# Kernel optimization log

Hardware: AMD Instinct MI355X
Metric: run time of the kernel (lower is better)

Reference implementation:

```python
import jax, jax.numpy as jnp
import numpy as np

BN_EPS = 1e-5


def gcn_conv(x, src, dst, ew, W, b, n_nodes):
    # PyG GCNConv: xW, then D^-1/2 (A+I) D^-1/2 aggregation (self-loop weight 1), then +bias
    xw = x @ W                                                  # [N, out]
    deg = jax.ops.segment_sum(ew, dst, num_segments=n_nodes) + 1.0  # includes self-loop
    dinv = jax.lax.rsqrt(deg)                                   # [N]
    norm = dinv[src] * ew * dinv[dst]                           # [E]
    agg = jax.ops.segment_sum(xw[src] * norm[:, None], dst, num_segments=n_nodes)
    agg = agg + xw * (1.0 / deg)[:, None]                       # self-loop term: dinv_i*1*dinv_i = 1/deg_i
    return agg + b


def batch_norm(h, gamma, beta):
    # training-mode BatchNorm1d: batch statistics (biased variance)
    mean = jnp.mean(h, axis=0)
    var = jnp.mean((h - mean) ** 2, axis=0)
    return (h - mean) * jax.lax.rsqrt(var + BN_EPS) * gamma + beta


def setup_inputs() -> dict:
    key = jax.random.key(0)
    ks = jax.random.split(key, 12)
    N, E, F_IN, H1, H2 = 100000, 1600000, 128, 64, 32
    x = jax.random.normal(ks[0], (N, F_IN), dtype=jnp.float32)
    edge_index = jax.random.randint(ks[1], (2, E), 0, N, dtype=jnp.int64)
    edge_weight = jax.random.uniform(ks[2], (E,), dtype=jnp.float32)
    W1 = jax.random.normal(ks[3], (F_IN, H1), dtype=jnp.float32) / np.sqrt(F_IN)
    b1 = jnp.zeros((H1,), dtype=jnp.float32)
    W2 = jax.random.normal(ks[4], (H1, H2), dtype=jnp.float32) / np.sqrt(H1)
    b2 = jnp.zeros((H2,), dtype=jnp.float32)
    g1 = jnp.ones((H1,), dtype=jnp.float32)
    be1 = jnp.zeros((H1,), dtype=jnp.float32)
    g2 = jnp.ones((H2,), dtype=jnp.float32)
    be2 = jnp.zeros((H2,), dtype=jnp.float32)
    Wl = jax.random.normal(ks[5], (H2, 1), dtype=jnp.float32) / np.sqrt(H2)
    bl = jnp.zeros((1,), dtype=jnp.float32)
    return {"x": x, "edge_index": edge_index, "edge_weight": edge_weight,
            "W1": W1, "b1": b1, "g1": g1, "be1": be1,
            "W2": W2, "b2": b2, "g2": g2, "be2": be2,
            "Wl": Wl, "bl": bl}


def reference(x, edge_index, edge_weight, W1, b1, g1, be1, W2, b2, g2, be2, Wl, bl):
    n_nodes = x.shape[0]
    src, dst = edge_index[0], edge_index[1]
    h = gcn_conv(x, src, dst, edge_weight, W1, b1, n_nodes)
    h = jax.nn.relu(batch_norm(h, g1, be1))          # dropout = identity (eval)
    h = gcn_conv(h, src, dst, edge_weight, W2, b2, n_nodes)
    h = jax.nn.relu(batch_norm(h, g2, be2))
    return (h @ Wl + bl).squeeze(-1)                 # [N]
```

## Files before the change

### kernel.cpp

```cpp
#include <hip/hip_runtime.h>
#include <hip/hip_bf16.h>

#define FIN 128
#define C1 64
#define C2 32
#define BN_EPS 1e-5f
#define CAP 28
#define OVFCAP 65536
#define R1 16
#define R2 16

typedef __hip_bfloat16 bf16;

__global__ __launch_bounds__(256) void k_fillpad(const int* __restrict__ ei, int* __restrict__ pcnt,
                                                 int* __restrict__ pad, int* __restrict__ ovf,
                                                 int* __restrict__ ovfn, int E) {
  int e = blockIdx.x * 256 + threadIdx.x;
  if (e < E) {
    int dst = ei[E + e];
    int pos = atomicAdd(&pcnt[dst], 1);
    if (pos < CAP) {
      pad[(size_t)dst * CAP + pos] = e;
    } else {
      int oi = atomicAdd(ovfn, 1);
      if (oi < OVFCAP) ovf[oi] = e;
    }
  }
}

__global__ __launch_bounds__(256) void k_ovfdeg(const int* __restrict__ ovf, const int* __restrict__ ovfn,
                                                const int* __restrict__ ei, const float* __restrict__ ew,
                                                float* __restrict__ deg, int E) {
  int n = ovfn[0];
  n = n < OVFCAP ? n : OVFCAP;
  for (int i = blockIdx.x * 256 + threadIdx.x; i < n; i += gridDim.x * 256) {
    int eid = ovf[i];
    atomicAdd(&deg[ei[E + eid]], ew[eid]);
  }
}

__global__ __launch_bounds__(256) void k_degdinv(const int* __restrict__ pcnt, const int* __restrict__ pad,
                                                 const float* __restrict__ ew, float* __restrict__ deg, int N) {
  int i = blockIdx.x * 256 + threadIdx.x;
  if (i < N) {
    int c = pcnt[i];
    c = c < CAP ? c : CAP;
    float s = deg[i] + 1.0f;
    const int* row = pad + (size_t)i * CAP;
    for (int k = 0; k < c; ++k) s += ew[row[k]];
    deg[i] = rsqrtf(s);
  }
}

__global__ __launch_bounds__(256) void k_gemm1(const float* __restrict__ x, const float* __restrict__ W1,
                                               bf16* __restrict__ xw1, int N) {
  const int lane = threadIdx.x & 63;
  const int w = threadIdx.x >> 6;
  float wr[32];
#pragma unroll
  for (int kk = 0; kk < 32; ++kk) wr[kk] = W1[(32 * w + kk) * C1 + lane];
  __shared__ float xs[R1][FIN];
  __shared__ float part[R1][4][C1];
  for (int base = blockIdx.x * R1; base < N; base += gridDim.x * R1) {
    int nrows = min(R1, N - base);
    __syncthreads();
    for (int t = threadIdx.x; t < nrows * FIN; t += 256) {
      int r = t >> 7, k = t & 127;
      xs[r][k] = x[(size_t)(base + r) * FIN + k];
    }
    __syncthreads();
#pragma unroll 4
    for (int r = 0; r < R1; ++r) {
      if (r >= nrows) break;
      const float* xrow = &xs[r][32 * w];
      float acc = 0.f;
#pragma unroll
      for (int kk = 0; kk < 32; kk += 4) {
        float4 xv = *(const float4*)&xrow[kk];
        acc = fmaf(xv.x, wr[kk], acc);
        acc = fmaf(xv.y, wr[kk + 1], acc);
        acc = fmaf(xv.z, wr[kk + 2], acc);
        acc = fmaf(xv.w, wr[kk + 3], acc);
      }
      part[r][w][lane] = acc;
    }
    __syncthreads();
    for (int t = threadIdx.x; t < nrows * C1; t += 256) {
      int r = t >> 6, c = t & 63;
      float v = (part[r][0][c] + part[r][1][c]) + (part[r][2][c] + part[r][3][c]);
      xw1[(size_t)(base + r) * C1 + c] = __float2bfloat16(v);
    }
  }
}

__global__ __launch_bounds__(256) void k_agg1(const int* __restrict__ pcnt, const int* __restrict__ pad,
                                              const int* __restrict__ ei, const float* __restrict__ ew,
                                              const float* __restrict__ dinv, const bf16* __restrict__ xw,
                                              const float* __restrict__ b, float* __restrict__ h, int N, int E) {
  const int lane = threadIdx.x & 63;
  const int wid = (blockIdx.x * 256 + threadIdx.x) >> 6;
  const int nw = (gridDim.x * 256) >> 6;
  for (int dst = wid; dst < N; dst += nw) {
    float dv = dinv[dst];
    float acc = fmaf(__bfloat162float(xw[(size_t)dst * C1 + lane]), dv * dv, b[lane]);
    int c = pcnt[dst];
    c = c < CAP ? c : CAP;
    int sv = 0;
    float nv = 0.f;
    if (lane < c) {
      int eid = pad[(size_t)dst * CAP + lane];
      sv = ei[eid];
      nv = dinv[sv] * ew[eid] * dv;
    }
    for (int k = 0; k < c; ++k) {
      int s = __shfl(sv, k);
      float nm = __shfl(nv, k);
      acc = fmaf(__bfloat162float(xw[(size_t)s * C1 + lane]), nm, acc);
    }
    h[(size_t)dst * C1 + lane] = acc;
  }
}

__global__ __launch_bounds__(256) void k_ovf1(const int* __restrict__ ovf, const int* __restrict__ ovfn,
                                              const int* __restrict__ ei, const float* __restrict__ ew,
                                              const float* __restrict__ dinv, const bf16* __restrict__ xw,
                                              float* __restrict__ h, int E) {
  const int lane = threadIdx.x & 63;
  const int wid = (blockIdx.x * 256 + threadIdx.x) >> 6;
  const int nw = (gridDim.x * 256) >> 6;
  int n = ovfn[0];
  n = n < OVFCAP ? n : OVFCAP;
  for (int i = wid; i < n; i += nw) {
    int eid = ovf[i];
    int src = ei[eid];
    int dst = ei[E + eid];
    float nrm = dinv[src] * ew[eid] * dinv[dst];
    atomicAdd(&h[(size_t)dst * C1 + lane], __bfloat162float(xw[(size_t)src * C1 + lane]) * nrm);
  }
}

__global__ __launch_bounds__(256) void k_agg2(const int* __restrict__ pcnt, const int* __restrict__ pad,
                                              const int* __restrict__ ei, const float* __restrict__ ew,
                                              const float* __restrict__ dinv, const float* __restrict__ xw,
                                              const float* __restrict__ b, float* __restrict__ h, int N, int E) {
  const int lane = threadIdx.x & 63;
  const int j = lane & 31, sub = lane >> 5;
  const int wid = (blockIdx.x * 256 + threadIdx.x) >> 6;
  const int nw = (gridDim.x * 256) >> 6;
  for (int dst = wid; dst < N; dst += nw) {
    float dv = dinv[dst];
    float acc = (sub == 0) ? fmaf(xw[(size_t)dst * C2 + j], dv * dv, b[j]) : 0.f;
    int c = pcnt[dst];
    c = c < CAP ? c : CAP;
    int sv = 0;
    float nv = 0.f;
    if (lane < c) {
      int eid = pad[(size_t)dst * CAP + lane];
      sv = ei[eid];
      nv = dinv[sv] * ew[eid] * dv;
    }
    for (int k = sub; k < c; k += 2) {
      int s = __shfl(sv, k);
      float nm = __shfl(nv, k);
      acc = fmaf(xw[(size_t)s * C2 + j], nm, acc);
    }
    acc += __shfl_xor(acc, 32);
    if (sub == 0) h[(size_t)dst * C2 + j] = acc;
  }
}

__global__ __launch_bounds__(256) void k_ovf2(const int* __restrict__ ovf, const int* __restrict__ ovfn,
                                              const int* __restrict__ ei, const float* __restrict__ ew,
                                              const float* __restrict__ dinv, const float* __restrict__ xw,
                                              float* __restrict__ h, int E) {
  const int lane = threadIdx.x & 63;
  const int wid = (blockIdx.x * 256 + threadIdx.x) >> 6;
  const int nw = (gridDim.x * 256) >> 6;
  int n = ovfn[0];
  n = n < OVFCAP ? n : OVFCAP;
  for (int i = wid; i < n; i += nw) {
    int eid = ovf[i];
    int src = ei[eid];
    int dst = ei[E + eid];
    float nrm = dinv[src] * ew[eid] * dinv[dst];
    if (lane < C2) atomicAdd(&h[(size_t)dst * C2 + lane], xw[(size_t)src * C2 + lane] * nrm);
  }
}

template <int C>
__global__ __launch_bounds__(256) void k_bnstats(const float* __restrict__ h, float* __restrict__ stat, int N) {
  const int rpb = 256 / C;
  const int j = threadIdx.x % C;
  const int rloc = threadIdx.x / C;
  float s = 0.f, sq = 0.f;
  for (int r = blockIdx.x * rpb + rloc; r < N; r += gridDim.x * rpb) {
    float v = h[(size_t)r * C + j];
    s += v;
    sq = fmaf(v, v, sq);
  }
  __shared__ float ls[256], lq[256];
  ls[threadIdx.x] = s;
  lq[threadIdx.x] = sq;
  __syncthreads();
  if (threadIdx.x < C) {
    float ts = 0.f, tq = 0.f;
#pragma unroll
    for (int k = 0; k < rpb; ++k) {
      ts += ls[k * C + j];
      tq += lq[k * C + j];
    }
    atomicAdd(&stat[j], ts);
    atomicAdd(&stat[C + j], tq);
  }
}

template <int C>
__global__ void k_bnfinal(const float* __restrict__ stat, const float* __restrict__ g,
                          const float* __restrict__ be, float* __restrict__ ss, int N) {
  int j = threadIdx.x;
  if (j < C) {
    float inv_n = 1.0f / (float)N;
    float mean = stat[j] * inv_n;
    float var = stat[C + j] * inv_n - mean * mean;
    float sc = g[j] * rsqrtf(var + BN_EPS);
    ss[j] = sc;
    ss[C + j] = be[j] - mean * sc;
  }
}

__global__ __launch_bounds__(256) void k_gemm2(const float* __restrict__ h1, const float* __restrict__ ss,
                                               const float* __restrict__ W2, float* __restrict__ xw2, int N) {
  const int lane = threadIdx.x & 63;
  const int w = threadIdx.x >> 6;
  const int c = lane & 31, hh = lane >> 5;
  const int slice = w * 2 + hh;
  float wr[8];
#pragma unroll
  for (int kk = 0; kk < 8; ++kk) wr[kk] = W2[(8 * slice + kk) * C2 + c];
  __shared__ float sss[2 * C1];
  if (threadIdx.x < 2 * C1) sss[threadIdx.x] = ss[threadIdx.x];
  __shared__ float xs[R2][C1];
  __shared__ float part[R2][8][C2];
  for (int base = blockIdx.x * R2; base < N; base += gridDim.x * R2) {
    int nrows = min(R2, N - base);
    __syncthreads();
    for (int t = threadIdx.x; t < nrows * C1; t += 256) {
      int r = t >> 6, k = t & 63;
      float v = fmaf(h1[(size_t)(base + r) * C1 + k], sss[k], sss[C1 + k]);
      xs[r][k] = v > 0.f ? v : 0.f;
    }
    __syncthreads();
#pragma unroll 4
    for (int r = 0; r < R2; ++r) {
      if (r >= nrows) break;
      const float* xrow = &xs[r][8 * slice];
      float4 a = *(const float4*)&xrow[0];
      float4 bb = *(const float4*)&xrow[4];
      float acc = a.x * wr[0];
      acc = fmaf(a.y, wr[1], acc);
      acc = fmaf(a.z, wr[2], acc);
      acc = fmaf(a.w, wr[3], acc);
      acc = fmaf(bb.x, wr[4], acc);
      acc = fmaf(bb.y, wr[5], acc);
      acc = fmaf(bb.z, wr[6], acc);
      acc = fmaf(bb.w, wr[7], acc);
      part[r][slice][c] = acc;
    }
    __syncthreads();
    for (int t = threadIdx.x; t < nrows * C2; t += 256) {
      int r = t >> 5, cc = t & 31;
      float v = 0.f;
#pragma unroll
      for (int s = 0; s < 8; ++s) v += part[r][s][cc];
      xw2[(size_t)(base + r) * C2 + cc] = v;
    }
  }
}

__global__ __launch_bounds__(256) void k_head(const float* __restrict__ h2, const float* __restrict__ ss,
                                              const float* __restrict__ Wl, const float* __restrict__ bl,
                                              float* __restrict__ out, int N) {
  const int lane = threadIdx.x & 63;
  const int j = lane & 31, sub = lane >> 5;
  const int wid = (blockIdx.x * 256 + threadIdx.x) >> 6;
  const int nw = (gridDim.x * 256) >> 6;
  const float sc = ss[j], sh = ss[C2 + j];
  const float wv = Wl[j];
  const float blv = bl[0];
  for (int r0 = wid * 2; r0 < N; r0 += nw * 2) {
    int row = r0 + sub;
    float v = 0.f;
    if (row < N) {
      float hh = fmaf(h2[(size_t)row * C2 + j], sc, sh);
      hh = hh > 0.f ? hh : 0.f;
      v = hh * wv;
    }
    v += __shfl_down(v, 16, 32);
    v += __shfl_down(v, 8, 32);
    v += __shfl_down(v, 4, 32);
    v += __shfl_down(v, 2, 32);
    v += __shfl_down(v, 1, 32);
    if (j == 0 && row < N) out[row] = v + blv;
  }
}

extern "C" void kernel_launch(void* const* d_in, const int* in_sizes, int n_in,
                              void* d_out, int out_size, void* d_ws, size_t ws_size,
                              hipStream_t stream) {
  const float* x = (const float*)d_in[0];
  const int* ei = (const int*)d_in[1];
  const float* ew = (const float*)d_in[2];
  const float* W1 = (const float*)d_in[3];
  const float* b1 = (const float*)d_in[4];
  const float* g1 = (const float*)d_in[5];
  const float* be1 = (const float*)d_in[6];
  const float* W2 = (const float*)d_in[7];
  const float* b2 = (const float*)d_in[8];
  const float* g2 = (const float*)d_in[9];
  const float* be2 = (const float*)d_in[10];
  const float* Wl = (const float*)d_in[11];
  const float* bl = (const float*)d_in[12];
  float* out = (float*)d_out;

  const int N = in_sizes[0] / FIN;
  const int E = in_sizes[2];

  float* Wf = (float*)d_ws;
  float* dinv = Wf;
  int* pcnt = (int*)(Wf + N);
  int* ovfn = (int*)(Wf + 2 * (size_t)N);
  float* stat1 = Wf + 2 * (size_t)N + 8;
  float* ss1 = stat1 + 128;
  float* stat2 = ss1 + 128;
  float* ss2 = stat2 + 64;
  int* ovf = (int*)(Wf + 2 * (size_t)N + 512);
  int* pad = ovf + OVFCAP;
  bf16* xw1 = (bf16*)(pad + (size_t)N * CAP);
  float* bufB = (float*)(xw1 + (size_t)N * C1);
  float* h1 = bufB;
  float* xw2 = (float*)xw1;
  float* h2 = bufB;

  hipMemsetAsync(Wf, 0, ((size_t)2 * N + 512) * sizeof(float), stream);

  k_fillpad<<<(E + 255) / 256, 256, 0, stream>>>(ei, pcnt, pad, ovf, ovfn, E);
  k_ovfdeg<<<16, 256, 0, stream>>>(ovf, ovfn, ei, ew, dinv, E);
  k_degdinv<<<(N + 255) / 256, 256, 0, stream>>>(pcnt, pad, ew, dinv, N);

  k_gemm1<<<2048, 256, 0, stream>>>(x, W1, xw1, N);
  k_agg1<<<4096, 256, 0, stream>>>(pcnt, pad, ei, ew, dinv, xw1, b1, h1, N, E);
  k_ovf1<<<256, 256, 0, stream>>>(ovf, ovfn, ei, ew, dinv, xw1, h1, E);
  k_bnstats<C1><<<1024, 256, 0, stream>>>(h1, stat1, N);
  k_bnfinal<C1><<<1, C1, 0, stream>>>(stat1, g1, be1, ss1, N);

  k_gemm2<<<2048, 256, 0, stream>>>(h1, ss1, W2, xw2, N);
  k_agg2<<<2048, 256, 0, stream>>>(pcnt, pad, ei, ew, dinv, xw2, b2, h2, N, E);
  k_ovf2<<<256, 256, 0, stream>>>(ovf, ovfn, ei, ew, dinv, xw2, h2, E);
  k_bnstats<C2><<<1024, 256, 0, stream>>>(h2, stat2, N);
  k_bnfinal<C2><<<1, C2, 0, stream>>>(stat2, g2, be2, ss2, N);

  k_head<<<1024, 256, 0, stream>>>(h2, ss2, Wl, bl, out, N);
}
```

Baseline: 650.7 us.

## Fuse edge bucketing with first GEMM and fold BN finalize into consumers

Merges the edge-to-destination padding kernel and the first dense GEMM into one launch, with disjoint block ranges doing each job so the atomic-heavy fill can overlap the compute-bound GEMM. The fill blocks now each scan all edges but only handle destinations in one of eight node ranges, which should improve atomic locality at the cost of reading the edge list eight times. The two single-block BN finalize kernels are removed, and the scale/shift computation is redone inside gemm2 and the head kernel, which saves launches but repeats a little work in every block.

```diff
diff --git a/kernel.cpp b/kernel.cpp
--- a/kernel.cpp
+++ b/kernel.cpp
@@ -9,21 +9,72 @@
 #define OVFCAP 65536
 #define R1 16
 #define R2 16
+#define GF 512
+#define GG 1024
 
 typedef __hip_bfloat16 bf16;
 
-__global__ __launch_bounds__(256) void k_fillpad(const int* __restrict__ ei, int* __restrict__ pcnt,
-                                                 int* __restrict__ pad, int* __restrict__ ovf,
-                                                 int* __restrict__ ovfn, int E) {
-  int e = blockIdx.x * 256 + threadIdx.x;
-  if (e < E) {
-    int dst = ei[E + e];
-    int pos = atomicAdd(&pcnt[dst], 1);
-    if (pos < CAP) {
-      pad[(size_t)dst * CAP + pos] = e;
-    } else {
-      int oi = atomicAdd(ovfn, 1);
-      if (oi < OVFCAP) ovf[oi] = e;
+__global__ __launch_bounds__(256) void k_fill_gemm1(const int* __restrict__ ei, int* __restrict__ pcnt,
+                                                    int* __restrict__ pad, int* __restrict__ ovf,
+                                                    int* __restrict__ ovfn,
+                                                    const float* __restrict__ x, const float* __restrict__ W1,
+                                                    bf16* __restrict__ xw1, int N, int E) {
+  __shared__ float xs[R1][FIN];
+  __shared__ float part[R1][4][C1];
+  if (blockIdx.x < GF) {
+    const int g = blockIdx.x & 7;
+    const int sub = blockIdx.x >> 3;
+    const int nsub = GF >> 3;
+    const int lo = (int)(((long long)N * g) >> 3);
+    const int hi = (int)(((long long)N * (g + 1)) >> 3);
+    for (int e = sub * 256 + threadIdx.x; e < E; e += nsub * 256) {
+      int dst = ei[E + e];
+      if (dst >= lo && dst < hi) {
+        int pos = atomicAdd(&pcnt[dst], 1);
+        if (pos < CAP) {
+          pad[(size_t)dst * CAP + pos] = e;
+        } else {
+          int oi = atomicAdd(ovfn, 1);
+          if (oi < OVFCAP) ovf[oi] = e;
+        }
+      }
+    }
+  } else {
+    const int bg = blockIdx.x - GF;
+    const int lane = threadIdx.x & 63;
+    const int w = threadIdx.x >> 6;
+    float wr[32];
+#pragma unroll
+    for (int kk = 0; kk < 32; ++kk) wr[kk] = W1[(32 * w + kk) * C1 + lane];
+    for (int base = bg * R1; base < N; base += GG * R1) {
+      int nrows = min(R1, N - base);
+      __syncthreads();
+      for (int t = threadIdx.x; t < nrows * FIN; t += 256) {
+        int r = t >> 7, k = t & 127;
+        xs[r][k] = x[(size_t)(base + r) * FIN + k];
+      }
+      __syncthreads();
+#pragma unroll 4
+      for (int r = 0; r < R1; ++r) {
+        if (r >= nrows) break;
+        const float* xrow = &xs[r][32 * w];
+        float acc = 0.f;
+#pragma unroll
+        for (int kk = 0; kk < 32; kk += 4) {
+          float4 xv = *(const float4*)&xrow[kk];
+          acc = fmaf(xv.x, wr[kk], acc);
+          acc = fmaf(xv.y, wr[kk + 1], acc);
+          acc = fmaf(xv.z, wr[kk + 2], acc);
+          acc = fmaf(xv.w, wr[kk + 3], acc);
+        }
+        part[r][w][lane] = acc;
+      }
+      __syncthreads();
+      for (int t = threadIdx.x; t < nrows * C1; t += 256) {
+        int r = t >> 6, c = t & 63;
+        float v = (part[r][0][c] + part[r][1][c]) + (part[r][2][c] + part[r][3][c]);
+        xw1[(size_t)(base + r) * C1 + c] = __float2bfloat16(v);
+      }
     }
   }
 }
@@ -49,47 +100,6 @@
     const int* row = pad + (size_t)i * CAP;
     for (int k = 0; k < c; ++k) s += ew[row[k]];
     deg[i] = rsqrtf(s);
-  }
-}
-
-__global__ __launch_bounds__(256) void k_gemm1(const float* __restrict__ x, const float* __restrict__ W1,
-                                               bf16* __restrict__ xw1, int N) {
-  const int lane = threadIdx.x & 63;
-  const int w = threadIdx.x >> 6;
-  float wr[32];
-#pragma unroll
-  for (int kk = 0; kk < 32; ++kk) wr[kk] = W1[(32 * w + kk) * C1 + lane];
-  __shared__ float xs[R1][FIN];
-  __shared__ float part[R1][4][C1];
-  for (int base = blockIdx.x * R1; base < N; base += gridDim.x * R1) {
-    int nrows = min(R1, N - base);
-    __syncthreads();
-    for (int t = threadIdx.x; t < nrows * FIN; t += 256) {
-      int r = t >> 7, k = t & 127;
-      xs[r][k] = x[(size_t)(base + r) * FIN + k];
-    }
-    __syncthreads();
-#pragma unroll 4
-    for (int r = 0; r < R1; ++r) {
-      if (r >= nrows) break;
-      const float* xrow = &xs[r][32 * w];
-      float acc = 0.f;
-#pragma unroll
-      for (int kk = 0; kk < 32; kk += 4) {
-        float4 xv = *(const float4*)&xrow[kk];
-        acc = fmaf(xv.x, wr[kk], acc);
-        acc = fmaf(xv.y, wr[kk + 1], acc);
-        acc = fmaf(xv.z, wr[kk + 2], acc);
-        acc = fmaf(xv.w, wr[kk + 3], acc);
-      }
-      part[r][w][lane] = acc;
-    }
-    __syncthreads();
-    for (int t = threadIdx.x; t < nrows * C1; t += 256) {
-      int r = t >> 6, c = t & 63;
-      float v = (part[r][0][c] + part[r][1][c]) + (part[r][2][c] + part[r][3][c]);
-      xw1[(size_t)(base + r) * C1 + c] = __float2bfloat16(v);
-    }
   }
 }
 
@@ -214,21 +224,8 @@
   }
 }
 
-template <int C>
-__global__ void k_bnfinal(const float* __restrict__ stat, const float* __restrict__ g,
-                          const float* __restrict__ be, float* __restrict__ ss, int N) {
-  int j = threadIdx.x;
-  if (j < C) {
-    float inv_n = 1.0f / (float)N;
-    float mean = stat[j] * inv_n;
-    float var = stat[C + j] * inv_n - mean * mean;
-    float sc = g[j] * rsqrtf(var + BN_EPS);
-    ss[j] = sc;
-    ss[C + j] = be[j] - mean * sc;
-  }
-}
-
-__global__ __launch_bounds__(256) void k_gemm2(const float* __restrict__ h1, const float* __restrict__ ss,
+__global__ __launch_bounds__(256) void k_gemm2(const float* __restrict__ h1, const float* __restrict__ stat,
+                                               const float* __restrict__ g, const float* __restrict__ be,
                                                const float* __restrict__ W2, float* __restrict__ xw2, int N) {
   const int lane = threadIdx.x & 63;
   const int w = threadIdx.x >> 6;
@@ -238,7 +235,14 @@
 #pragma unroll
   for (int kk = 0; kk < 8; ++kk) wr[kk] = W2[(8 * slice + kk) * C2 + c];
   __shared__ float sss[2 * C1];
-  if (threadIdx.x < 2 * C1) sss[threadIdx.x] = ss[threadIdx.x];
+  if (threadIdx.x < C1) {
+    float inv_n = 1.0f / (float)N;
+    float mean = stat[threadIdx.x] * inv_n;
+    float var = stat[C1 + threadIdx.x] * inv_n - mean * mean;
+    float sc = g[threadIdx.x] * rsqrtf(var + BN_EPS);
+    sss[threadIdx.x] = sc;
+    sss[C1 + threadIdx.x] = be[threadIdx.x] - mean * sc;
+  }
   __shared__ float xs[R2][C1];
   __shared__ float part[R2][8][C2];
   for (int base = blockIdx.x * R2; base < N; base += gridDim.x * R2) {
@@ -277,14 +281,19 @@
   }
 }
 
-__global__ __launch_bounds__(256) void k_head(const float* __restrict__ h2, const float* __restrict__ ss,
+__global__ __launch_bounds__(256) void k_head(const float* __restrict__ h2, const float* __restrict__ stat,
+                                              const float* __restrict__ g, const float* __restrict__ be,
                                               const float* __restrict__ Wl, const float* __restrict__ bl,
                                               float* __restrict__ out, int N) {
   const int lane = threadIdx.x & 63;
   const int j = lane & 31, sub = lane >> 5;
   const int wid = (blockIdx.x * 256 + threadIdx.x) >> 6;
   const int nw = (gridDim.x * 256) >> 6;
-  const float sc = ss[j], sh = ss[C2 + j];
+  const float inv_n = 1.0f / (float)N;
+  const float mean = stat[j] * inv_n;
+  const float var = stat[C2 + j] * inv_n - mean * mean;
+  const float sc = g[j] * rsqrtf(var + BN_EPS);
+  const float sh = be[j] - mean * sc;
   const float wv = Wl[j];
   const float blv = bl[0];
   for (int r0 = wid * 2; r0 < N; r0 += nw * 2) {
@@ -330,9 +339,7 @@
   int* pcnt = (int*)(Wf + N);
   int* ovfn = (int*)(Wf + 2 * (size_t)N);
   float* stat1 = Wf + 2 * (size_t)N + 8;
-  float* ss1 = stat1 + 128;
-  float* stat2 = ss1 + 128;
-  float* ss2 = stat2 + 64;
+  float* stat2 = stat1 + 128;
   int* ovf = (int*)(Wf + 2 * (size_t)N + 512);
   int* pad = ovf + OVFCAP;
   bf16* xw1 = (bf16*)(pad + (size_t)N * CAP);
@@ -343,21 +350,18 @@
 
   hipMemsetAsync(Wf, 0, ((size_t)2 * N + 512) * sizeof(float), stream);
 
-  k_fillpad<<<(E + 255) / 256, 256, 0, stream>>>(ei, pcnt, pad, ovf, ovfn, E);
+  k_fill_gemm1<<<GF + GG, 256, 0, stream>>>(ei, pcnt, pad, ovf, ovfn, x, W1, xw1, N, E);
   k_ovfdeg<<<16, 256, 0, stream>>>(ovf, ovfn, ei, ew, dinv, E);
   k_degdinv<<<(N + 255) / 256, 256, 0, stream>>>(pcnt, pad, ew, dinv, N);
 
-  k_gemm1<<<2048, 256, 0, stream>>>(x, W1, xw1, N);
   k_agg1<<<4096, 256, 0, stream>>>(pcnt, pad, ei, ew, dinv, xw1, b1, h1, N, E);
   k_ovf1<<<256, 256, 0, stream>>>(ovf, ovfn, ei, ew, dinv, xw1, h1, E);
   k_bnstats<C1><<<1024, 256, 0, stream>>>(h1, stat1, N);
-  k_bnfinal<C1><<<1, C1, 0, stream>>>(stat1, g1, be1, ss1, N);
-
-  k_gemm2<<<2048, 256, 0, stream>>>(h1, ss1, W2, xw2, N);
+
+  k_gemm2<<<2048, 256, 0, stream>>>(h1, stat1, g1, be1, W2, xw2, N);
   k_agg2<<<2048, 256, 0, stream>>>(pcnt, pad, ei, ew, dinv, xw2, b2, h2, N, E);
   k_ovf2<<<256, 256, 0, stream>>>(ovf, ovfn, ei, ew, dinv, xw2, h2, E);
   k_bnstats<C2><<<1024, 256, 0, stream>>>(h2, stat2, N);
-  k_bnfinal<C2><<<1, C2, 0, stream>>>(stat2, g2, be2, ss2, N);
-
-  k_head<<<1024, 256, 0, stream>>>(h2, ss2, Wl, bl, out, N);
-}
+
+  k_head<<<1024, 256, 0, stream>>>(h2, stat2, g2, be2, Wl, bl, out, N);
+}
```

Result: faster. 571.1 us (-12.2%).
